# Optimization experiments

Hardware: AMD Instinct MI355X
Metric: run time of the kernel (lower is better)

Reference implementation:

```python
import jax, jax.numpy as jnp
import numpy as np

N_VERT = 100000
N_EDGE = 50000
NNZ = 3200000
IN_CH = 256
OUT_CH = 64


def setup_inputs() -> dict:
    key = jax.random.key(0)
    k1, k2, k3, k4, k5, k6 = jax.random.split(key, 6)
    X = jax.random.normal(k1, (N_VERT, IN_CH), dtype=jnp.float32)
    W = jax.random.normal(k2, (OUT_CH, IN_CH), dtype=jnp.float32) * (IN_CH ** -0.5)
    degE = jax.random.uniform(k3, (N_EDGE,), dtype=jnp.float32, minval=0.01, maxval=1.0)
    degV = jax.random.uniform(k4, (N_VERT,), dtype=jnp.float32, minval=0.01, maxval=1.0)
    Wdiag = jnp.ones((N_EDGE,), dtype=jnp.float32)
    v_idx = jax.random.randint(k5, (NNZ,), 0, N_VERT, dtype=jnp.int32)
    e_idx = jax.random.randint(k6, (NNZ,), 0, N_EDGE, dtype=jnp.int32)
    return {"X": X, "W": W, "degE": degE, "degV": degV, "Wdiag": Wdiag,
            "v_idx": v_idx, "e_idx": e_idx}


def reference(X, W, degE, degV, Wdiag, v_idx, e_idx):
    # Dense projection: [N, in] @ [in, out] -> [N, out]
    Xp = jnp.einsum('ni,oi->no', X, W)
    # Stage 1: vertex -> hyperedge aggregation, degE + Wdiag normalization
    Xe = jax.ops.segment_sum(Xp[v_idx], e_idx, num_segments=N_EDGE)
    Xe = Xe * (degE * Wdiag)[:, None]
    # Stage 2: hyperedge -> vertex aggregation, degV normalization
    Xv = jax.ops.segment_sum(Xe[e_idx], v_idx, num_segments=N_VERT)
    Xv = Xv * degV[:, None]
    return Xv
```

## Files before the change

### kernel.cpp

```cpp
#include <hip/hip_runtime.h>

#define NV   100000
#define NE   50000
#define NNZ  3200000
#define KIN  256
#define KOUT 64

#define NB    128
#define CHUNK (NNZ / NB)
#define NBE   782
#define NBV   1563
#define NBINS (NBE + NBV)
#define LSCAN (NBINS * NB)
#define NBLK_SCAN ((LSCAN + 1023) / 1024)

#define ECAP_E 6144
#define ECAP_V 4096

typedef short short8 __attribute__((ext_vector_type(8)));
typedef float f32x4  __attribute__((ext_vector_type(4)));

__device__ __forceinline__ unsigned short f2bf(float f) {
    union { float f; unsigned u; } c{f};
    const unsigned lsb = (c.u >> 16) & 1u;
    return (unsigned short)((c.u + 0x7FFFu + lsb) >> 16);
}
__device__ __forceinline__ float bf2f_lo(unsigned u) {
    union { unsigned u; float f; } c{u << 16};
    return c.f;
}
__device__ __forceinline__ float bf2f_hi(unsigned u) {
    union { unsigned u; float f; } c{u & 0xFFFF0000u};
    return c.f;
}
__device__ __forceinline__ short8 pack8(const float4 lo, const float4 hi) {
    short8 r;
    r[0] = (short)f2bf(lo.x); r[1] = (short)f2bf(lo.y);
    r[2] = (short)f2bf(lo.z); r[3] = (short)f2bf(lo.w);
    r[4] = (short)f2bf(hi.x); r[5] = (short)f2bf(hi.y);
    r[6] = (short)f2bf(hi.z); r[7] = (short)f2bf(hi.w);
    return r;
}

__global__ __launch_bounds__(256) void k_wb(const float* __restrict__ W,
                                            unsigned short* __restrict__ Wb) {
    const int i = blockIdx.x * 256 + threadIdx.x;
    Wb[i] = f2bf(W[i]);
}

__global__ __launch_bounds__(256) void k_project(const float* __restrict__ X,
                                                 const unsigned short* __restrict__ Wb,
                                                 unsigned short* __restrict__ Xpb) {
    const int tid  = threadIdx.x;
    const int lane = tid & 63;
    const int wv   = tid >> 6;
    const int l15  = lane & 15;
    const int l4   = lane >> 4;
    const int rbase = blockIdx.x * 128 + wv * 32;

    const int r0 = min(rbase + l15,      NV - 1);
    const int r1 = min(rbase + 16 + l15, NV - 1);
    const float* xp0 = X + (size_t)r0 * KIN + l4 * 8;
    const float* xp1 = X + (size_t)r1 * KIN + l4 * 8;
    const unsigned short* wp = Wb + (size_t)l15 * KIN + l4 * 8;

    f32x4 acc[2][4];
#pragma unroll
    for (int t = 0; t < 2; ++t)
#pragma unroll
        for (int g = 0; g < 4; ++g)
            acc[t][g] = (f32x4){0.f, 0.f, 0.f, 0.f};

#pragma unroll
    for (int s = 0; s < 8; ++s) {
        const int k0 = s * 32;
        const float4 a0lo = *(const float4*)(xp0 + k0);
        const float4 a0hi = *(const float4*)(xp0 + k0 + 4);
        const float4 a1lo = *(const float4*)(xp1 + k0);
        const float4 a1hi = *(const float4*)(xp1 + k0 + 4);
        short8 b[4];
#pragma unroll
        for (int g = 0; g < 4; ++g)
            b[g] = *(const short8*)(wp + (size_t)g * 16 * KIN + k0);
        const short8 a0 = pack8(a0lo, a0hi);
        const short8 a1 = pack8(a1lo, a1hi);
#pragma unroll
        for (int g = 0; g < 4; ++g) {
            acc[0][g] = __builtin_amdgcn_mfma_f32_16x16x32_bf16(a0, b[g], acc[0][g], 0, 0, 0);
            acc[1][g] = __builtin_amdgcn_mfma_f32_16x16x32_bf16(a1, b[g], acc[1][g], 0, 0, 0);
        }
    }

#pragma unroll
    for (int t = 0; t < 2; ++t)
#pragma unroll
        for (int i = 0; i < 4; ++i) {
            const int r = rbase + t * 16 + l4 * 4 + i;
            if (r < NV) {
#pragma unroll
                for (int g = 0; g < 4; ++g)
                    Xpb[(size_t)r * KOUT + g * 16 + l15] = f2bf(acc[t][g][i]);
            }
        }
}

__global__ __launch_bounds__(1024) void k_hist(const int* __restrict__ v_idx,
                                               const int* __restrict__ e_idx,
                                               int* __restrict__ mat) {
    __shared__ int h[NBINS];
    const int b = blockIdx.x, tid = threadIdx.x;
    for (int i = tid; i < NBINS; i += 1024) h[i] = 0;
    __syncthreads();
    const int base = b * CHUNK;
    for (int i = tid; i < CHUNK; i += 1024) {
        atomicAdd(&h[e_idx[base + i] >> 6], 1);
        atomicAdd(&h[NBE + (v_idx[base + i] >> 6)], 1);
    }
    __syncthreads();
    for (int j = tid; j < NBINS; j += 1024) mat[j * NB + b] = h[j];
}

__global__ __launch_bounds__(1024) void k_scan1(int* __restrict__ mat,
                                                int* __restrict__ bsum) {
    __shared__ int buf[1024];
    const int tid = threadIdx.x;
    const int i = blockIdx.x * 1024 + tid;
    const int v = (i < LSCAN) ? mat[i] : 0;
    buf[tid] = v;
    __syncthreads();
    for (int d = 1; d < 1024; d <<= 1) {
        int t = (tid >= d) ? buf[tid - d] : 0;
        __syncthreads();
        buf[tid] += t;
        __syncthreads();
    }
    if (i < LSCAN) mat[i] = buf[tid] - v;
    if (tid == 1023) bsum[blockIdx.x] = buf[1023];
}

__global__ __launch_bounds__(1024) void k_scan2(int* __restrict__ bsum) {
    __shared__ int buf[1024];
    const int tid = threadIdx.x;
    const int v = (tid < NBLK_SCAN) ? bsum[tid] : 0;
    buf[tid] = v;
    __syncthreads();
    for (int d = 1; d < 1024; d <<= 1) {
        int t = (tid >= d) ? buf[tid - d] : 0;
        __syncthreads();
        buf[tid] += t;
        __syncthreads();
    }
    if (tid < NBLK_SCAN) bsum[tid] = buf[tid] - v;
}

__global__ __launch_bounds__(1024) void k_scan3(int* __restrict__ mat,
                                                const int* __restrict__ bsum) {
    const int i = blockIdx.x * 1024 + threadIdx.x;
    if (i < LSCAN) mat[i] += bsum[blockIdx.x];
}

__global__ __launch_bounds__(1024) void k_partition2(const int* __restrict__ v_idx,
                                                     const int* __restrict__ e_idx,
                                                     const int* __restrict__ mat,
                                                     unsigned* __restrict__ partE,
                                                     unsigned* __restrict__ partV) {
    __shared__ int curE[NBE];
    __shared__ int curV[NBV];
    const int b = blockIdx.x, tid = threadIdx.x;
    for (int j = tid; j < NBE; j += 1024) curE[j] = mat[j * NB + b];
    for (int j = tid; j < NBV; j += 1024) curV[j] = mat[(NBE + j) * NB + b] - NNZ;
    __syncthreads();
    const int base = b * CHUNK;
    for (int i = tid; i < CHUNK; i += 1024) {
        const int v = v_idx[base + i];
        const int e = e_idx[base + i];
        const int pE = atomicAdd(&curE[e >> 6], 1);
        partE[pE] = (unsigned)v | ((unsigned)(e & 63) << 17);
        const int pV = atomicAdd(&curV[v >> 6], 1);
        partV[pV] = (unsigned)e | ((unsigned)(v & 63) << 17);
    }
}

__global__ __launch_bounds__(1024) void k_sortgatherE(const unsigned* __restrict__ part,
                                                      const int* __restrict__ mat,
                                                      const unsigned short* __restrict__ Xpb,
                                                      const float* __restrict__ degE,
                                                      const float* __restrict__ Wdiag,
                                                      unsigned short* __restrict__ Xeb) {
    __shared__ unsigned sbuf[ECAP_E];
    __shared__ int hist[64], cur[64], pfx[65];
    const int b = blockIdx.x, tid = threadIdx.x;
    const int base = mat[b * NB];
    const int end  = (b == NBE - 1) ? NNZ : mat[(b + 1) * NB];
    const int nb = end - base;

    if (tid < 64) hist[tid] = 0;
    __syncthreads();
    for (int i = tid; i < nb; i += 1024)
        atomicAdd(&hist[(part[base + i] >> 17) & 63], 1);
    __syncthreads();
    if (tid == 0) {
        int s = 0;
        for (int k = 0; k < 64; ++k) { pfx[k] = s; cur[k] = s; s += hist[k]; }
        pfx[64] = s;
    }
    __syncthreads();
    for (int i = tid; i < nb; i += 1024) {
        const unsigned u = part[base + i];
        const int p = atomicAdd(&cur[(u >> 17) & 63], 1);
        sbuf[p] = u & 0x1FFFFu;
    }
    __syncthreads();

    const int wv = tid >> 6, lane = tid & 63;
    const int q = lane >> 4, sl = lane & 15;
#pragma unroll
    for (int j = 0; j < 4; ++j) {
        const int le = wv * 4 + j;
        const int e_id = (b << 6) + le;
        const int s0 = pfx[le];
        const int n  = pfx[le + 1] - s0;
        float a0 = 0.f, a1 = 0.f, a2 = 0.f, a3 = 0.f;
        const int nf = n >> 2;
        int t = 0;
        for (; t + 4 <= nf; t += 4) {
            int idx[4]; uint2 u4[4];
#pragma unroll
            for (int z = 0; z < 4; ++z) idx[z] = (int)sbuf[s0 + 4 * (t + z) + q];
#pragma unroll
            for (int z = 0; z < 4; ++z)
                u4[z] = *(const uint2*)&Xpb[(size_t)idx[z] * KOUT + 4 * sl];
#pragma unroll
            for (int z = 0; z < 4; ++z) {
                a0 += bf2f_lo(u4[z].x); a1 += bf2f_hi(u4[z].x);
                a2 += bf2f_lo(u4[z].y); a3 += bf2f_hi(u4[z].y);
            }
        }
        for (; t < nf; ++t) {
            const int idx = (int)sbuf[s0 + 4 * t + q];
            const uint2 u = *(const uint2*)&Xpb[(size_t)idx * KOUT + 4 * sl];
            a0 += bf2f_lo(u.x); a1 += bf2f_hi(u.x);
            a2 += bf2f_lo(u.y); a3 += bf2f_hi(u.y);
        }
        if (n & 3) {
            const int src = nf * 4 + q;
            if (src < n) {
                const int idx = (int)sbuf[s0 + src];
                const uint2 u = *(const uint2*)&Xpb[(size_t)idx * KOUT + 4 * sl];
                a0 += bf2f_lo(u.x); a1 += bf2f_hi(u.x);
                a2 += bf2f_lo(u.y); a3 += bf2f_hi(u.y);
            }
        }
        a0 += __shfl_xor(a0, 16, 64); a0 += __shfl_xor(a0, 32, 64);
        a1 += __shfl_xor(a1, 16, 64); a1 += __shfl_xor(a1, 32, 64);
        a2 += __shfl_xor(a2, 16, 64); a2 += __shfl_xor(a2, 32, 64);
        a3 += __shfl_xor(a3, 16, 64); a3 += __shfl_xor(a3, 32, 64);
        if (q == 0 && e_id < NE) {
            const float s = degE[e_id] * Wdiag[e_id];
            uint2 pk;
            pk.x = (unsigned)f2bf(a0 * s) | ((unsigned)f2bf(a1 * s) << 16);
            pk.y = (unsigned)f2bf(a2 * s) | ((unsigned)f2bf(a3 * s) << 16);
            *(uint2*)&Xeb[(size_t)e_id * KOUT + 4 * sl] = pk;
        }
    }
}

__global__ __launch_bounds__(1024) void k_sortgatherV(const unsigned* __restrict__ part,
                                                      const int* __restrict__ mat,
                                                      const unsigned short* __restrict__ Xeb,
                                                      const float* __restrict__ degV,
                                                      float* __restrict__ out) {
    __shared__ unsigned sbuf[ECAP_V];
    __shared__ int hist[64], cur[64], pfx[65];
    const int b = blockIdx.x, tid = threadIdx.x;
    const int base = mat[NBE * NB + b * NB] - NNZ;
    const int end  = (b == NBV - 1) ? NNZ : (mat[NBE * NB + (b + 1) * NB] - NNZ);
    const int nb = end - base;

    if (tid < 64) hist[tid] = 0;
    __syncthreads();
    for (int i = tid; i < nb; i += 1024)
        atomicAdd(&hist[(part[base + i] >> 17) & 63], 1);
    __syncthreads();
    if (tid == 0) {
        int s = 0;
        for (int k = 0; k < 64; ++k) { pfx[k] = s; cur[k] = s; s += hist[k]; }
        pfx[64] = s;
    }
    __syncthreads();
    for (int i = tid; i < nb; i += 1024) {
        const unsigned u = part[base + i];
        const int p = atomicAdd(&cur[(u >> 17) & 63], 1);
        sbuf[p] = u & 0x1FFFFu;
    }
    __syncthreads();

    const int wv = tid >> 6, lane = tid & 63;
    const int q = lane >> 4, sl = lane & 15;
#pragma unroll
    for (int j = 0; j < 4; ++j) {
        const int lv = wv * 4 + j;
        const int v_id = (b << 6) + lv;
        const int s0 = pfx[lv];
        const int n  = pfx[lv + 1] - s0;
        float a0 = 0.f, a1 = 0.f, a2 = 0.f, a3 = 0.f;
        const int nf = n >> 2;
        int t = 0;
        for (; t + 4 <= nf; t += 4) {
            int idx[4]; uint2 u4[4];
#pragma unroll
            for (int z = 0; z < 4; ++z) idx[z] = (int)sbuf[s0 + 4 * (t + z) + q];
#pragma unroll
            for (int z = 0; z < 4; ++z)
                u4[z] = *(const uint2*)&Xeb[(size_t)idx[z] * KOUT + 4 * sl];
#pragma unroll
            for (int z = 0; z < 4; ++z) {
                a0 += bf2f_lo(u4[z].x); a1 += bf2f_hi(u4[z].x);
                a2 += bf2f_lo(u4[z].y); a3 += bf2f_hi(u4[z].y);
            }
        }
        for (; t < nf; ++t) {
            const int idx = (int)sbuf[s0 + 4 * t + q];
            const uint2 u = *(const uint2*)&Xeb[(size_t)idx * KOUT + 4 * sl];
            a0 += bf2f_lo(u.x); a1 += bf2f_hi(u.x);
            a2 += bf2f_lo(u.y); a3 += bf2f_hi(u.y);
        }
        if (n & 3) {
            const int src = nf * 4 + q;
            if (src < n) {
                const int idx = (int)sbuf[s0 + src];
                const uint2 u = *(const uint2*)&Xeb[(size_t)idx * KOUT + 4 * sl];
                a0 += bf2f_lo(u.x); a1 += bf2f_hi(u.x);
                a2 += bf2f_lo(u.y); a3 += bf2f_hi(u.y);
            }
        }
        a0 += __shfl_xor(a0, 16, 64); a0 += __shfl_xor(a0, 32, 64);
        a1 += __shfl_xor(a1, 16, 64); a1 += __shfl_xor(a1, 32, 64);
        a2 += __shfl_xor(a2, 16, 64); a2 += __shfl_xor(a2, 32, 64);
        a3 += __shfl_xor(a3, 16, 64); a3 += __shfl_xor(a3, 32, 64);
        if (q == 0 && v_id < NV) {
            const float s = degV[v_id];
            *(float4*)&out[(size_t)v_id * KOUT + 4 * sl] =
                make_float4(a0 * s, a1 * s, a2 * s, a3 * s);
        }
    }
}

extern "C" void kernel_launch(void* const* d_in, const int* in_sizes, int n_in,
                              void* d_out, int out_size, void* d_ws, size_t ws_size,
                              hipStream_t stream) {
    const float* X     = (const float*)d_in[0];
    const float* W     = (const float*)d_in[1];
    const float* degE  = (const float*)d_in[2];
    const float* degV  = (const float*)d_in[3];
    const float* Wdiag = (const float*)d_in[4];
    const int*   v_idx = (const int*)d_in[5];
    const int*   e_idx = (const int*)d_in[6];
    float* out = (float*)d_out;

    unsigned short* Xpb  = (unsigned short*)d_ws;
    unsigned short* Xeb  = Xpb + (size_t)NV * KOUT;
    unsigned*       partE = (unsigned*)(Xeb + (size_t)NE * KOUT);
    unsigned*       partV = partE + NNZ;
    int*            mat   = (int*)(partV + NNZ);
    int*            bsum  = mat + LSCAN;
    unsigned short* Wb    = (unsigned short*)(bsum + ((NBLK_SCAN + 3) & ~3));

    k_wb<<<(KIN * KOUT) / 256, 256, 0, stream>>>(W, Wb);
    k_project<<<(NV + 127) / 128, 256, 0, stream>>>(X, Wb, Xpb);

    k_hist<<<NB, 1024, 0, stream>>>(v_idx, e_idx, mat);
    k_scan1<<<NBLK_SCAN, 1024, 0, stream>>>(mat, bsum);
    k_scan2<<<1, 1024, 0, stream>>>(bsum);
    k_scan3<<<NBLK_SCAN, 1024, 0, stream>>>(mat, bsum);

    k_partition2<<<NB, 1024, 0, stream>>>(v_idx, e_idx, mat, partE, partV);

    k_sortgatherE<<<NBE, 1024, 0, stream>>>(partE, mat, Xpb, degE, Wdiag, Xeb);
    k_sortgatherV<<<NBV, 1024, 0, stream>>>(partV, mat, Xeb, degV, out);
}
```

Baseline: 244.0 us.

## Write-combine partition scatter via LDS staging and pad buckets to 8-aligned

Replaces the single fused partition kernel with two per-side kernels. Each stages scattered entries per bucket in shared memory and flushes full 8-entry sections as 32-byte vector stores, with a fallback to direct writes. Bucket starts are padded to multiples of 8 by a new scan kernel. The V side now uses 128-vertex buckets, which halves the vertex bucket count and makes each sort-gather block handle 8 vertices per wave. The aim is coalesced global writes in place of random 4-byte scatters, paid for with extra syncs, more shared memory and two passes over the indices.

```diff
diff --git a/kernel.cpp b/kernel.cpp
--- a/kernel.cpp
+++ b/kernel.cpp
@@ -6,16 +6,17 @@
 #define KIN  256
 #define KOUT 64
 
-#define NB    128
-#define CHUNK (NNZ / NB)
-#define NBE   782
-#define NBV   1563
-#define NBINS (NBE + NBV)
-#define LSCAN (NBINS * NB)
+#define NBL   64
+#define CHUNK (NNZ / NBL)
+#define NBKT  782
+#define NBINS (2 * NBKT)
+#define LSCAN (NBINS * NBL)
 #define NBLK_SCAN ((LSCAN + 1023) / 1024)
 
 #define ECAP_E 6144
-#define ECAP_V 4096
+#define ECAP_V 4608
+#define PCAP  (NNZ + 8192)
+#define FINF  0x7FFFFFFF
 
 typedef short short8 __attribute__((ext_vector_type(8)));
 typedef float f32x4  __attribute__((ext_vector_type(4)));
@@ -114,10 +115,10 @@
     const int base = b * CHUNK;
     for (int i = tid; i < CHUNK; i += 1024) {
         atomicAdd(&h[e_idx[base + i] >> 6], 1);
-        atomicAdd(&h[NBE + (v_idx[base + i] >> 6)], 1);
-    }
-    __syncthreads();
-    for (int j = tid; j < NBINS; j += 1024) mat[j * NB + b] = h[j];
+        atomicAdd(&h[NBKT + (v_idx[base + i] >> 7)], 1);
+    }
+    __syncthreads();
+    for (int j = tid; j < NBINS; j += 1024) mat[j * NBL + b] = h[j];
 }
 
 __global__ __launch_bounds__(1024) void k_scan1(int* __restrict__ mat,
@@ -159,30 +160,121 @@
     if (i < LSCAN) mat[i] += bsum[blockIdx.x];
 }
 
-__global__ __launch_bounds__(1024) void k_partition2(const int* __restrict__ v_idx,
-                                                     const int* __restrict__ e_idx,
-                                                     const int* __restrict__ mat,
-                                                     unsigned* __restrict__ partE,
-                                                     unsigned* __restrict__ partV) {
-    __shared__ int curE[NBE];
-    __shared__ int curV[NBV];
+__global__ __launch_bounds__(1024) void k_pad(const int* __restrict__ mat,
+                                              int* __restrict__ psE,
+                                              int* __restrict__ psV) {
+    __shared__ int buf[1024];
+    const int tid = threadIdx.x;
+    int c = 0;
+    if (tid < NBKT) {
+        const int s = mat[tid * NBL];
+        const int e = (tid == NBKT - 1) ? NNZ : mat[(tid + 1) * NBL];
+        c = (e - s + 7) & ~7;
+    }
+    buf[tid] = c;
+    __syncthreads();
+    for (int d = 1; d < 1024; d <<= 1) {
+        int t = (tid >= d) ? buf[tid - d] : 0;
+        __syncthreads();
+        buf[tid] += t;
+        __syncthreads();
+    }
+    if (tid < NBKT) psE[tid] = buf[tid] - c;
+    __syncthreads();
+    c = 0;
+    if (tid < NBKT) {
+        const int s = mat[(NBKT + tid) * NBL];
+        const int e = (tid == NBKT - 1) ? 2 * NNZ : mat[(NBKT + tid + 1) * NBL];
+        c = (e - s + 7) & ~7;
+    }
+    buf[tid] = c;
+    __syncthreads();
+    for (int d = 1; d < 1024; d <<= 1) {
+        int t = (tid >= d) ? buf[tid - d] : 0;
+        __syncthreads();
+        buf[tid] += t;
+        __syncthreads();
+    }
+    if (tid < NBKT) psV[tid] = buf[tid] - c;
+}
+
+template <int SIDE>
+__global__ __launch_bounds__(1024) void k_partwc(const int* __restrict__ v_idx,
+                                                 const int* __restrict__ e_idx,
+                                                 const int* __restrict__ mat,
+                                                 const int* __restrict__ ps,
+                                                 unsigned* __restrict__ part) {
+    __shared__ int pos[NBKT], fsec[NBKT];
+    __shared__ unsigned char bad[NBKT];
+    __shared__ unsigned stg[NBKT * 16];
     const int b = blockIdx.x, tid = threadIdx.x;
-    for (int j = tid; j < NBE; j += 1024) curE[j] = mat[j * NB + b];
-    for (int j = tid; j < NBV; j += 1024) curV[j] = mat[(NBE + j) * NB + b] - NNZ;
-    __syncthreads();
+    const int jOff = SIDE ? NBKT : 0;
+
+    for (int j = tid; j < NBKT; j += 1024) {
+        const int p = ps[j] + (mat[(jOff + j) * NBL + b] - mat[(jOff + j) * NBL]);
+        pos[j] = p;
+        fsec[j] = (p + 7) >> 3;
+        bad[j] = 0;
+    }
+    __syncthreads();
+
     const int base = b * CHUNK;
-    for (int i = tid; i < CHUNK; i += 1024) {
-        const int v = v_idx[base + i];
-        const int e = e_idx[base + i];
-        const int pE = atomicAdd(&curE[e >> 6], 1);
-        partE[pE] = (unsigned)v | ((unsigned)(e & 63) << 17);
-        const int pV = atomicAdd(&curV[v >> 6], 1);
-        partV[pV] = (unsigned)e | ((unsigned)(v & 63) << 17);
+    for (int t0 = 0; t0 < CHUNK; t0 += 1024) {
+        if (t0 + tid < CHUNK) {
+            const int i = base + t0 + tid;
+            const int v = v_idx[i], e = e_idx[i];
+            int j; unsigned val;
+            if (SIDE == 0) { j = e >> 6; val = (unsigned)v | ((unsigned)(e & 63) << 17); }
+            else           { j = v >> 7; val = (unsigned)e | ((unsigned)(v & 127) << 16); }
+            const int g = atomicAdd(&pos[j], 1);
+            const int sec = g >> 3;
+            const int fs = fsec[j];
+            if (fs != FINF && sec >= fs && sec <= fs + 1) {
+                stg[j * 16 + (sec & 1) * 8 + (g & 7)] = val;
+                if (bad[j]) part[g] = val;
+            } else {
+                part[g] = val;
+                if (fs != FINF && sec > fs + 1) bad[j] = 1;
+            }
+        }
+        __syncthreads();
+        if (tid < NBKT) {
+            const int j = tid;
+            int fs = fsec[j];
+            if (fs != FINF) {
+                if (!bad[j]) {
+                    const int lim = pos[j] >> 3;
+                    while (fs < lim) {
+                        uint4* dst = (uint4*)&part[fs << 3];
+                        const unsigned* s = &stg[j * 16 + (fs & 1) * 8];
+                        dst[0] = make_uint4(s[0], s[1], s[2], s[3]);
+                        dst[1] = make_uint4(s[4], s[5], s[6], s[7]);
+                        ++fs;
+                    }
+                    fsec[j] = fs;
+                } else {
+                    const int hi = min(pos[j], (fs + 2) << 3);
+                    for (int g = fs << 3; g < hi; ++g)
+                        part[g] = stg[j * 16 + ((g >> 3) & 1) * 8 + (g & 7)];
+                    fsec[j] = FINF;
+                }
+            }
+        }
+        __syncthreads();
+    }
+    if (tid < NBKT) {
+        const int j = tid;
+        const int fs = fsec[j];
+        if (fs != FINF && !bad[j]) {
+            for (int g = fs << 3; g < pos[j]; ++g)
+                part[g] = stg[j * 16 + ((g >> 3) & 1) * 8 + (g & 7)];
+        }
     }
 }
 
 __global__ __launch_bounds__(1024) void k_sortgatherE(const unsigned* __restrict__ part,
                                                       const int* __restrict__ mat,
+                                                      const int* __restrict__ psE,
                                                       const unsigned short* __restrict__ Xpb,
                                                       const float* __restrict__ degE,
                                                       const float* __restrict__ Wdiag,
@@ -190,9 +282,8 @@
     __shared__ unsigned sbuf[ECAP_E];
     __shared__ int hist[64], cur[64], pfx[65];
     const int b = blockIdx.x, tid = threadIdx.x;
-    const int base = mat[b * NB];
-    const int end  = (b == NBE - 1) ? NNZ : mat[(b + 1) * NB];
-    const int nb = end - base;
+    const int base = psE[b];
+    const int nb = ((b == NBKT - 1) ? NNZ : mat[(b + 1) * NBL]) - mat[b * NBL];
 
     if (tid < 64) hist[tid] = 0;
     __syncthreads();
@@ -267,40 +358,40 @@
 
 __global__ __launch_bounds__(1024) void k_sortgatherV(const unsigned* __restrict__ part,
                                                       const int* __restrict__ mat,
+                                                      const int* __restrict__ psV,
                                                       const unsigned short* __restrict__ Xeb,
                                                       const float* __restrict__ degV,
                                                       float* __restrict__ out) {
     __shared__ unsigned sbuf[ECAP_V];
-    __shared__ int hist[64], cur[64], pfx[65];
+    __shared__ int hist[128], cur[128], pfx[129];
     const int b = blockIdx.x, tid = threadIdx.x;
-    const int base = mat[NBE * NB + b * NB] - NNZ;
-    const int end  = (b == NBV - 1) ? NNZ : (mat[NBE * NB + (b + 1) * NB] - NNZ);
-    const int nb = end - base;
-
-    if (tid < 64) hist[tid] = 0;
+    const int base = psV[b];
+    const int nb = ((b == NBKT - 1) ? 2 * NNZ : mat[(NBKT + b + 1) * NBL]) - mat[(NBKT + b) * NBL];
+
+    if (tid < 128) hist[tid] = 0;
     __syncthreads();
     for (int i = tid; i < nb; i += 1024)
-        atomicAdd(&hist[(part[base + i] >> 17) & 63], 1);
+        atomicAdd(&hist[(part[base + i] >> 16) & 127], 1);
     __syncthreads();
     if (tid == 0) {
         int s = 0;
-        for (int k = 0; k < 64; ++k) { pfx[k] = s; cur[k] = s; s += hist[k]; }
-        pfx[64] = s;
+        for (int k = 0; k < 128; ++k) { pfx[k] = s; cur[k] = s; s += hist[k]; }
+        pfx[128] = s;
     }
     __syncthreads();
     for (int i = tid; i < nb; i += 1024) {
         const unsigned u = part[base + i];
-        const int p = atomicAdd(&cur[(u >> 17) & 63], 1);
-        sbuf[p] = u & 0x1FFFFu;
+        const int p = atomicAdd(&cur[(u >> 16) & 127], 1);
+        sbuf[p] = u & 0xFFFFu;
     }
     __syncthreads();
 
     const int wv = tid >> 6, lane = tid & 63;
     const int q = lane >> 4, sl = lane & 15;
 #pragma unroll
-    for (int j = 0; j < 4; ++j) {
-        const int lv = wv * 4 + j;
-        const int v_id = (b << 6) + lv;
+    for (int j = 0; j < 8; ++j) {
+        const int lv = wv * 8 + j;
+        const int v_id = (b << 7) + lv;
         const int s0 = pfx[lv];
         const int n  = pfx[lv + 1] - s0;
         float a0 = 0.f, a1 = 0.f, a2 = 0.f, a3 = 0.f;
@@ -361,21 +452,25 @@
     unsigned short* Xpb  = (unsigned short*)d_ws;
     unsigned short* Xeb  = Xpb + (size_t)NV * KOUT;
     unsigned*       partE = (unsigned*)(Xeb + (size_t)NE * KOUT);
-    unsigned*       partV = partE + NNZ;
-    int*            mat   = (int*)(partV + NNZ);
+    unsigned*       partV = partE + PCAP;
+    int*            mat   = (int*)(partV + PCAP);
     int*            bsum  = mat + LSCAN;
-    unsigned short* Wb    = (unsigned short*)(bsum + ((NBLK_SCAN + 3) & ~3));
+    int*            psE   = bsum + 128;
+    int*            psV   = psE + NBKT;
+    unsigned short* Wb    = (unsigned short*)(psV + NBKT);
 
     k_wb<<<(KIN * KOUT) / 256, 256, 0, stream>>>(W, Wb);
     k_project<<<(NV + 127) / 128, 256, 0, stream>>>(X, Wb, Xpb);
 
-    k_hist<<<NB, 1024, 0, stream>>>(v_idx, e_idx, mat);
+    k_hist<<<NBL, 1024, 0, stream>>>(v_idx, e_idx, mat);
     k_scan1<<<NBLK_SCAN, 1024, 0, stream>>>(mat, bsum);
     k_scan2<<<1, 1024, 0, stream>>>(bsum);
     k_scan3<<<NBLK_SCAN, 1024, 0, stream>>>(mat, bsum);
-
-    k_partition2<<<NB, 1024, 0, stream>>>(v_idx, e_idx, mat, partE, partV);
-
-    k_sortgatherE<<<NBE, 1024, 0, stream>>>(partE, mat, Xpb, degE, Wdiag, Xeb);
-    k_sortgatherV<<<NBV, 1024, 0, stream>>>(partV, mat, Xeb, degV, out);
-}
+    k_pad<<<1, 1024, 0, stream>>>(mat, psE, psV);
+
+    k_partwc<0><<<NBL, 1024, 0, stream>>>(v_idx, e_idx, mat, psE, partE);
+    k_partwc<1><<<NBL, 1024, 0, stream>>>(v_idx, e_idx, mat, psV, partV);
+
+    k_sortgatherE<<<NBKT, 1024, 0, stream>>>(partE, mat, psE, Xpb, degE, Wdiag, Xeb);
+    k_sortgatherV<<<NBKT, 1024, 0, stream>>>(partV, mat, psV, Xeb, degV, out);
+}
```

After: 304.8 us. +24.9%, slower.

## Fuse histogram into projection kernel and widen gather loads to 16 bytes

Applied to the files above, without the earlier changes.

The histogram pass now runs inside the first NB blocks of the projection kernel, with 256 threads per block instead of 1024, which removes one launch and lets the histogram overlap with the GEMM. The two sort-gather kernels now have each lane load 8 bf16 values (uint4) instead of 4. That halves the lanes per row and doubles the rows handled in parallel per wavefront, at the cost of more accumulator registers and an extra shuffle-reduction step. The fused histogram blocks carry more work with fewer threads and could become stragglers that delay the projection kernel's completion.

```diff
diff --git a/kernel.cpp b/kernel.cpp
--- a/kernel.cpp
+++ b/kernel.cpp
@@ -50,13 +50,22 @@
 
 __global__ __launch_bounds__(256) void k_project(const float* __restrict__ X,
                                                  const unsigned short* __restrict__ Wb,
-                                                 unsigned short* __restrict__ Xpb) {
+                                                 unsigned short* __restrict__ Xpb,
+                                                 const int* __restrict__ v_idx,
+                                                 const int* __restrict__ e_idx,
+                                                 int* __restrict__ mat) {
+    __shared__ int h[NBINS];
     const int tid  = threadIdx.x;
     const int lane = tid & 63;
     const int wv   = tid >> 6;
     const int l15  = lane & 15;
     const int l4   = lane >> 4;
     const int rbase = blockIdx.x * 128 + wv * 32;
+
+    const bool doHist = (blockIdx.x < NB);
+    if (doHist) {
+        for (int i = tid; i < NBINS; i += 256) h[i] = 0;
+    }
 
     const int r0 = min(rbase + l15,      NV - 1);
     const int r1 = min(rbase + 16 + l15, NV - 1);
@@ -102,22 +111,17 @@
                     Xpb[(size_t)r * KOUT + g * 16 + l15] = f2bf(acc[t][g][i]);
             }
         }
-}
-
-__global__ __launch_bounds__(1024) void k_hist(const int* __restrict__ v_idx,
-                                               const int* __restrict__ e_idx,
-                                               int* __restrict__ mat) {
-    __shared__ int h[NBINS];
-    const int b = blockIdx.x, tid = threadIdx.x;
-    for (int i = tid; i < NBINS; i += 1024) h[i] = 0;
-    __syncthreads();
-    const int base = b * CHUNK;
-    for (int i = tid; i < CHUNK; i += 1024) {
-        atomicAdd(&h[e_idx[base + i] >> 6], 1);
-        atomicAdd(&h[NBE + (v_idx[base + i] >> 6)], 1);
-    }
-    __syncthreads();
-    for (int j = tid; j < NBINS; j += 1024) mat[j * NB + b] = h[j];
+
+    if (doHist) {
+        __syncthreads();
+        const int base = blockIdx.x * CHUNK;
+        for (int i = tid; i < CHUNK; i += 256) {
+            atomicAdd(&h[e_idx[base + i] >> 6], 1);
+            atomicAdd(&h[NBE + (v_idx[base + i] >> 6)], 1);
+        }
+        __syncthreads();
+        for (int j = tid; j < NBINS; j += 256) mat[j * NB + blockIdx.x] = h[j];
+    }
 }
 
 __global__ __launch_bounds__(1024) void k_scan1(int* __restrict__ mat,
@@ -213,54 +217,66 @@
     __syncthreads();
 
     const int wv = tid >> 6, lane = tid & 63;
-    const int q = lane >> 4, sl = lane & 15;
+    const int q = lane >> 3, sl = lane & 7;
 #pragma unroll
     for (int j = 0; j < 4; ++j) {
         const int le = wv * 4 + j;
         const int e_id = (b << 6) + le;
         const int s0 = pfx[le];
         const int n  = pfx[le + 1] - s0;
-        float a0 = 0.f, a1 = 0.f, a2 = 0.f, a3 = 0.f;
-        const int nf = n >> 2;
+        float a0 = 0.f, a1 = 0.f, a2 = 0.f, a3 = 0.f,
+              a4 = 0.f, a5 = 0.f, a6 = 0.f, a7 = 0.f;
+        const int nf = n >> 3;
         int t = 0;
         for (; t + 4 <= nf; t += 4) {
-            int idx[4]; uint2 u4[4];
-#pragma unroll
-            for (int z = 0; z < 4; ++z) idx[z] = (int)sbuf[s0 + 4 * (t + z) + q];
+            int idx[4]; uint4 u4[4];
+#pragma unroll
+            for (int z = 0; z < 4; ++z) idx[z] = (int)sbuf[s0 + 8 * (t + z) + q];
 #pragma unroll
             for (int z = 0; z < 4; ++z)
-                u4[z] = *(const uint2*)&Xpb[(size_t)idx[z] * KOUT + 4 * sl];
+                u4[z] = *(const uint4*)&Xpb[(size_t)idx[z] * KOUT + 8 * sl];
 #pragma unroll
             for (int z = 0; z < 4; ++z) {
                 a0 += bf2f_lo(u4[z].x); a1 += bf2f_hi(u4[z].x);
                 a2 += bf2f_lo(u4[z].y); a3 += bf2f_hi(u4[z].y);
+                a4 += bf2f_lo(u4[z].z); a5 += bf2f_hi(u4[z].z);
+                a6 += bf2f_lo(u4[z].w); a7 += bf2f_hi(u4[z].w);
             }
         }
         for (; t < nf; ++t) {
-            const int idx = (int)sbuf[s0 + 4 * t + q];
-            const uint2 u = *(const uint2*)&Xpb[(size_t)idx * KOUT + 4 * sl];
+            const int idx = (int)sbuf[s0 + 8 * t + q];
+            const uint4 u = *(const uint4*)&Xpb[(size_t)idx * KOUT + 8 * sl];
             a0 += bf2f_lo(u.x); a1 += bf2f_hi(u.x);
             a2 += bf2f_lo(u.y); a3 += bf2f_hi(u.y);
-        }
-        if (n & 3) {
-            const int src = nf * 4 + q;
+            a4 += bf2f_lo(u.z); a5 += bf2f_hi(u.z);
+            a6 += bf2f_lo(u.w); a7 += bf2f_hi(u.w);
+        }
+        if (n & 7) {
+            const int src = nf * 8 + q;
             if (src < n) {
                 const int idx = (int)sbuf[s0 + src];
-                const uint2 u = *(const uint2*)&Xpb[(size_t)idx * KOUT + 4 * sl];
+                const uint4 u = *(const uint4*)&Xpb[(size_t)idx * KOUT + 8 * sl];
                 a0 += bf2f_lo(u.x); a1 += bf2f_hi(u.x);
                 a2 += bf2f_lo(u.y); a3 += bf2f_hi(u.y);
+                a4 += bf2f_lo(u.z); a5 += bf2f_hi(u.z);
+                a6 += bf2f_lo(u.w); a7 += bf2f_hi(u.w);
             }
         }
-        a0 += __shfl_xor(a0, 16, 64); a0 += __shfl_xor(a0, 32, 64);
-        a1 += __shfl_xor(a1, 16, 64); a1 += __shfl_xor(a1, 32, 64);
-        a2 += __shfl_xor(a2, 16, 64); a2 += __shfl_xor(a2, 32, 64);
-        a3 += __shfl_xor(a3, 16, 64); a3 += __shfl_xor(a3, 32, 64);
+#pragma unroll
+        for (int d = 8; d < 64; d <<= 1) {
+            a0 += __shfl_xor(a0, d, 64); a1 += __shfl_xor(a1, d, 64);
+            a2 += __shfl_xor(a2, d, 64); a3 += __shfl_xor(a3, d, 64);
+            a4 += __shfl_xor(a4, d, 64); a5 += __shfl_xor(a5, d, 64);
+            a6 += __shfl_xor(a6, d, 64); a7 += __shfl_xor(a7, d, 64);
+        }
         if (q == 0 && e_id < NE) {
             const float s = degE[e_id] * Wdiag[e_id];
-            uint2 pk;
+            uint4 pk;
             pk.x = (unsigned)f2bf(a0 * s) | ((unsigned)f2bf(a1 * s) << 16);
             pk.y = (unsigned)f2bf(a2 * s) | ((unsigned)f2bf(a3 * s) << 16);
-            *(uint2*)&Xeb[(size_t)e_id * KOUT + 4 * sl] = pk;
+            pk.z = (unsigned)f2bf(a4 * s) | ((unsigned)f2bf(a5 * s) << 16);
+            pk.w = (unsigned)f2bf(a6 * s) | ((unsigned)f2bf(a7 * s) << 16);
+            *(uint4*)&Xeb[(size_t)e_id * KOUT + 8 * sl] = pk;
         }
     }
 }
@@ -296,52 +312,64 @@
     __syncthreads();
 
     const int wv = tid >> 6, lane = tid & 63;
-    const int q = lane >> 4, sl = lane & 15;
+    const int q = lane >> 3, sl = lane & 7;
 #pragma unroll
     for (int j = 0; j < 4; ++j) {
         const int lv = wv * 4 + j;
         const int v_id = (b << 6) + lv;
         const int s0 = pfx[lv];
         const int n  = pfx[lv + 1] - s0;
-        float a0 = 0.f, a1 = 0.f, a2 = 0.f, a3 = 0.f;
-        const int nf = n >> 2;
+        float a0 = 0.f, a1 = 0.f, a2 = 0.f, a3 = 0.f,
+              a4 = 0.f, a5 = 0.f, a6 = 0.f, a7 = 0.f;
+        const int nf = n >> 3;
         int t = 0;
         for (; t + 4 <= nf; t += 4) {
-            int idx[4]; uint2 u4[4];
-#pragma unroll
-            for (int z = 0; z < 4; ++z) idx[z] = (int)sbuf[s0 + 4 * (t + z) + q];
+            int idx[4]; uint4 u4[4];
+#pragma unroll
+            for (int z = 0; z < 4; ++z) idx[z] = (int)sbuf[s0 + 8 * (t + z) + q];
 #pragma unroll
             for (int z = 0; z < 4; ++z)
-                u4[z] = *(const uint2*)&Xeb[(size_t)idx[z] * KOUT + 4 * sl];
+                u4[z] = *(const uint4*)&Xeb[(size_t)idx[z] * KOUT + 8 * sl];
 #pragma unroll
             for (int z = 0; z < 4; ++z) {
                 a0 += bf2f_lo(u4[z].x); a1 += bf2f_hi(u4[z].x);
                 a2 += bf2f_lo(u4[z].y); a3 += bf2f_hi(u4[z].y);
+                a4 += bf2f_lo(u4[z].z); a5 += bf2f_hi(u4[z].z);
+                a6 += bf2f_lo(u4[z].w); a7 += bf2f_hi(u4[z].w);
             }
         }
         for (; t < nf; ++t) {
-            const int idx = (int)sbuf[s0 + 4 * t + q];
-            const uint2 u = *(const uint2*)&Xeb[(size_t)idx * KOUT + 4 * sl];
+            const int idx = (int)sbuf[s0 + 8 * t + q];
+            const uint4 u = *(const uint4*)&Xeb[(size_t)idx * KOUT + 8 * sl];
             a0 += bf2f_lo(u.x); a1 += bf2f_hi(u.x);
             a2 += bf2f_lo(u.y); a3 += bf2f_hi(u.y);
-        }
-        if (n & 3) {
-            const int src = nf * 4 + q;
+            a4 += bf2f_lo(u.z); a5 += bf2f_hi(u.z);
+            a6 += bf2f_lo(u.w); a7 += bf2f_hi(u.w);
+        }
+        if (n & 7) {
+            const int src = nf * 8 + q;
             if (src < n) {
                 const int idx = (int)sbuf[s0 + src];
-                const uint2 u = *(const uint2*)&Xeb[(size_t)idx * KOUT + 4 * sl];
+                const uint4 u = *(const uint4*)&Xeb[(size_t)idx * KOUT + 8 * sl];
                 a0 += bf2f_lo(u.x); a1 += bf2f_hi(u.x);
                 a2 += bf2f_lo(u.y); a3 += bf2f_hi(u.y);
+                a4 += bf2f_lo(u.z); a5 += bf2f_hi(u.z);
+                a6 += bf2f_lo(u.w); a7 += bf2f_hi(u.w);
             }
         }
-        a0 += __shfl_xor(a0, 16, 64); a0 += __shfl_xor(a0, 32, 64);
-        a1 += __shfl_xor(a1, 16, 64); a1 += __shfl_xor(a1, 32, 64);
-        a2 += __shfl_xor(a2, 16, 64); a2 += __shfl_xor(a2, 32, 64);
-        a3 += __shfl_xor(a3, 16, 64); a3 += __shfl_xor(a3, 32, 64);
+#pragma unroll
+        for (int d = 8; d < 64; d <<= 1) {
+            a0 += __shfl_xor(a0, d, 64); a1 += __shfl_xor(a1, d, 64);
+            a2 += __shfl_xor(a2, d, 64); a3 += __shfl_xor(a3, d, 64);
+            a4 += __shfl_xor(a4, d, 64); a5 += __shfl_xor(a5, d, 64);
+            a6 += __shfl_xor(a6, d, 64); a7 += __shfl_xor(a7, d, 64);
+        }
         if (q == 0 && v_id < NV) {
             const float s = degV[v_id];
-            *(float4*)&out[(size_t)v_id * KOUT + 4 * sl] =
+            *(float4*)&out[(size_t)v_id * KOUT + 8 * sl] =
                 make_float4(a0 * s, a1 * s, a2 * s, a3 * s);
+            *(float4*)&out[(size_t)v_id * KOUT + 8 * sl + 4] =
+                make_float4(a4 * s, a5 * s, a6 * s, a7 * s);
         }
     }
 }
@@ -367,9 +395,8 @@
     unsigned short* Wb    = (unsigned short*)(bsum + ((NBLK_SCAN + 3) & ~3));
 
     k_wb<<<(KIN * KOUT) / 256, 256, 0, stream>>>(W, Wb);
-    k_project<<<(NV + 127) / 128, 256, 0, stream>>>(X, Wb, Xpb);
-
-    k_hist<<<NB, 1024, 0, stream>>>(v_idx, e_idx, mat);
+    k_project<<<(NV + 127) / 128, 256, 0, stream>>>(X, Wb, Xpb, v_idx, e_idx, mat);
+
     k_scan1<<<NBLK_SCAN, 1024, 0, stream>>>(mat, bsum);
     k_scan2<<<1, 1024, 0, stream>>>(bsum);
     k_scan3<<<NBLK_SCAN, 1024, 0, stream>>>(mat, bsum);
```

Result: slower. 266.8 us (+9.3%).
